# Optimization experiments

Measured on AMD Instinct MI355X. Metric: run time of the kernel, lower is better.

Reference implementation:

```python
import jax, jax.numpy as jnp
import numpy as np

B, T, C = 32, 512, 1024
H, D = 16, 64
BLOCK_SIZE = 512


def setup_inputs() -> dict:
    key = jax.random.key(0)
    ks = jax.random.split(key, 6)
    s_in = 1.0 / np.sqrt(C)
    return {
        "x": jax.random.normal(ks[0], (B, T, C), dtype=jnp.float32),
        "wq": jax.random.normal(ks[1], (H, C, D), dtype=jnp.float32) * s_in,
        "wk": jax.random.normal(ks[2], (H, C, D), dtype=jnp.float32) * s_in,
        "wv": jax.random.normal(ks[3], (H, C, D), dtype=jnp.float32) * s_in,
        "w_proj": jax.random.normal(ks[4], (C, C), dtype=jnp.float32) * s_in,
        "b_proj": jax.random.normal(ks[5], (C,), dtype=jnp.float32) * 0.01,
    }


def reference(x, wq, wk, wv, w_proj, b_proj):
    b, t, c = x.shape
    # per-head projections (bias=False Linears stacked on head axis)
    q = jnp.einsum("btc,hcd->bhtd", x, wq)
    k = jnp.einsum("btc,hcd->bhtd", x, wk)
    v = jnp.einsum("btc,hcd->bhtd", x, wv)
    # NOTE: original scales by 1/sqrt(C) with C = n_embd, not head_size
    scale = 1.0 / (c ** 0.5)
    scores = jnp.einsum("bhtd,bhsd->bhts", q, k) * scale  # [B,H,T,T]
    causal = jnp.tril(jnp.ones((t, t), dtype=bool))
    scores = jnp.where(causal, scores, jnp.finfo(scores.dtype).min)
    attn = jax.nn.softmax(scores, axis=-1)
    out = jnp.einsum("bhts,bhsd->bhtd", attn, v)
    # concat heads in order -> [B,T,H*D]
    out = out.transpose(0, 2, 1, 3).reshape(b, t, -1)
    # output projection (dropout = identity in eval mode)
    return out @ w_proj + b_proj
```

## Files before the change

kernel.cpp:

```cpp
#include <hip/hip_runtime.h>

typedef unsigned int u32;
typedef unsigned short u16;
typedef __bf16 bf16x8 __attribute__((ext_vector_type(8)));
typedef float f32x4 __attribute__((ext_vector_type(4)));
typedef u16 u16x8 __attribute__((ext_vector_type(8)));
typedef u16 u16x4 __attribute__((ext_vector_type(4)));

#define DEVI static __device__ __forceinline__

DEVI u16 f2bf(float f) {
  union { float f; u32 u; } v; v.f = f;
  return (u16)((v.u + 0x7fffu + ((v.u >> 16) & 1u)) >> 16);
}

DEVI u32 cvtpk(float a, float b) {
  u32 r;
  asm("v_cvt_pk_bf16_f32 %0, %1, %2" : "=v"(r) : "v"(a), "v"(b));
  return r;
}

constexpr long QS_ = 16777216;
constexpr long XB_O    = 0;
constexpr long WQKV_O  = 16777216;
constexpr long Q_O     = 19922944;
constexpr long CTX_O   = 70254592;
constexpr long WPROJ_O = 87031808;

__global__ __launch_bounds__(256) void k_cast_x(const float* __restrict__ x, u16* __restrict__ xb) {
  long i = (long)blockIdx.x * 256 + threadIdx.x;
  const float4* p = (const float4*)(x + i * 8);
  float4 a = p[0], b = p[1];
  u16x8 r;
  r[0]=f2bf(a.x); r[1]=f2bf(a.y); r[2]=f2bf(a.z); r[3]=f2bf(a.w);
  r[4]=f2bf(b.x); r[5]=f2bf(b.y); r[6]=f2bf(b.z); r[7]=f2bf(b.w);
  *(u16x8*)(xb + i * 8) = r;
}

__global__ __launch_bounds__(256) void k_prep_wqkv(const float* __restrict__ wq, const float* __restrict__ wk,
                                                   const float* __restrict__ wv, u16* __restrict__ wt) {
  long o = (long)blockIdx.x * 256 + threadIdx.x;
  int n = (int)(o >> 10), kk = (int)(o & 1023);
  int sel = n >> 10, h = (n >> 6) & 15, d = n & 63;
  const float* W = (sel == 0) ? wq : ((sel == 1) ? wk : wv);
  wt[o] = f2bf(W[((long)h * 1024 + kk) * 64 + d]);
}

__global__ __launch_bounds__(256) void k_prep_wproj(const float* __restrict__ wp, u16* __restrict__ wt) {
  long o = (long)blockIdx.x * 256 + threadIdx.x;
  int n = (int)(o >> 10), kk = (int)(o & 1023);
  wt[o] = f2bf(wp[(long)kk * 1024 + n]);
}

DEVI void gload16(const u16* g, u16* l) {
  __builtin_amdgcn_global_load_lds((const __attribute__((address_space(1))) u32*)g,
                                   (__attribute__((address_space(3))) u32*)l, 16, 0, 0);
}

template <int NN, int EPI>
__global__ __launch_bounds__(512, 2)
void k_gemm(const u16* __restrict__ A, const u16* __restrict__ Bt,
            u16* __restrict__ oq, float* __restrict__ of, const float* __restrict__ bias) {
  __shared__ u16 lds[2][4][8192];

  const int tid = threadIdx.x;
  const int lane = tid & 63;
  const int w = tid >> 6;
  const int wm = w >> 2, wn = w & 3;
  const int lg = lane >> 4, lr = lane & 15;
  const int bht = 2 + (wn >> 1);
  const int bn0 = (wn & 1) * 4;

  constexpr int NBN = NN / 256;
  const int nwg = gridDim.x;
  const int swz = ((int)blockIdx.x & 7) * (nwg >> 3) + ((int)blockIdx.x >> 3);
  const long m0 = (long)(swz / NBN) * 256, n0 = (long)(swz % NBN) * 256;

  int srcoff[2];
  #pragma unroll
  for (int r2 = 0; r2 < 2; ++r2) {
    int s = r2 * 8 + w;
    int mi = s >> 1, ks = s & 1;
    int rowl = mi * 16 + (lane >> 2);
    int colu = ks * 32 + (((lane & 3) * 8) ^ (((lane >> 5) & 1) * 16));
    srcoff[r2] = rowl * 1024 + colu;
  }
  const int fo = lr * 32 + ((lg * 8) ^ (((lr >> 3) & 1) * 16));

  const u16* At  = A  + m0 * 1024;
  const u16* Bt2 = Bt + n0 * 1024;

  f32x4 acc[8][4] = {};
  bf16x8 aq[2][2][2];
  bf16x8 bfr[4][2];

#define STAGE(buf_, ht_, gbase_)                                               \
  { _Pragma("unroll") for (int r_ = 0; r_ < 2; ++r_)                           \
      gload16((gbase_) + srcoff[r_], &lds[buf_][ht_][r_ * 4096 + w * 512]); }

#define LDS_AQ(set_, buf_, q_)                                                 \
  { _Pragma("unroll") for (int i_ = 0; i_ < 2; ++i_)                           \
    _Pragma("unroll") for (int ks_ = 0; ks_ < 2; ++ks_)                        \
      aq[set_][i_][ks_] = *(const bf16x8*)&lds[buf_][wm][(((q_)*2 + i_) * 2 + ks_) * 512 + fo]; }

#define LDS_BF(buf_, lo_)                                                      \
  { _Pragma("unroll") for (int j_ = 0; j_ < 2; ++j_)                           \
    _Pragma("unroll") for (int ks_ = 0; ks_ < 2; ++ks_)                        \
      bfr[(lo_) + j_][ks_] = *(const bf16x8*)&lds[buf_][bht][((bn0 + (lo_) + j_) * 2 + ks_) * 512 + fo]; }

#define QUAD8(set_, q_, lo_)                                                   \
  { __builtin_amdgcn_s_setprio(1);                                             \
    _Pragma("unroll") for (int ks_ = 0; ks_ < 2; ++ks_)                        \
    _Pragma("unroll") for (int i_ = 0; i_ < 2; ++i_)                           \
    _Pragma("unroll") for (int j_ = 0; j_ < 2; ++j_)                           \
      acc[(q_)*2 + i_][(lo_) + j_] = __builtin_amdgcn_mfma_f32_16x16x32_bf16(  \
          aq[set_][i_][ks_], bfr[(lo_) + j_][ks_], acc[(q_)*2 + i_][(lo_) + j_], 0, 0, 0); \
    __builtin_amdgcn_s_setprio(0); }

#define BARF() { asm volatile("s_barrier" ::: "memory"); }

  STAGE(0, 0, At);
  STAGE(0, 1, At + 131072);
  STAGE(0, 2, Bt2);
  STAGE(0, 3, Bt2 + 131072);
  STAGE(1, 0, At + 64);
  STAGE(1, 1, At + 131072 + 64);
  STAGE(1, 2, Bt2 + 64);
  STAGE(1, 3, Bt2 + 131072 + 64);
  asm volatile("s_waitcnt vmcnt(8)" ::: "memory");
  BARF();
  LDS_AQ(0, 0, 0);
  LDS_BF(0, 0);

  #pragma unroll 1
  for (int t = 0; t < 16; ++t) {
    const int buf = t & 1;
    LDS_BF(buf, 2);
    LDS_AQ(1, buf, 1);
    QUAD8(0, 0, 0);
    BARF();
    QUAD8(0, 0, 2);
    BARF();
    LDS_AQ(0, buf, 2);
    if (t + 2 < 16) { STAGE(buf, 2, Bt2 + (t + 2) * 64); STAGE(buf, 3, Bt2 + 131072 + (t + 2) * 64); }
    QUAD8(1, 1, 0);
    BARF();
    QUAD8(1, 1, 2);
    BARF();
    LDS_AQ(1, buf, 3);
    QUAD8(0, 2, 0);
    BARF();
    QUAD8(0, 2, 2);
    asm volatile("s_waitcnt lgkmcnt(0)" ::: "memory");
    __builtin_amdgcn_sched_barrier(0);
    BARF();
    if (t + 2 < 16) { STAGE(buf, 0, At + (t + 2) * 64); STAGE(buf, 1, At + 131072 + (t + 2) * 64); }
    QUAD8(1, 3, 0);
    BARF();
    if (t < 14)       { asm volatile("s_waitcnt vmcnt(8)" ::: "memory"); }
    else if (t == 14) { asm volatile("s_waitcnt vmcnt(0)" ::: "memory"); }
    BARF();
    if (t + 1 < 16) {
      LDS_AQ(0, buf ^ 1, 0);
      LDS_BF(buf ^ 1, 0);
    }
    QUAD8(1, 3, 2);
    BARF();
  }

  if constexpr (EPI == 0) {
    #pragma unroll
    for (int mi = 0; mi < 8; ++mi) {
      int grow = (int)m0 + wm * 128 + mi * 16 + lg * 4;
      int b = grow >> 9, t0 = grow & 511;
      #pragma unroll
      for (int ni = 0; ni < 4; ++ni) {
        int gcol = (int)n0 + wn * 64 + ni * 16 + lr;
        int sel = gcol >> 10, h = (gcol >> 6) & 15, d = gcol & 63;
        u16* dst = oq + (long)sel * QS_ + (((long)(b * 16 + h) * 512 + t0) * 64 + d);
        #pragma unroll
        for (int r = 0; r < 4; ++r) dst[r * 64] = f2bf(acc[mi][ni][r]);
      }
    }
  } else {
    float bv[4];
    #pragma unroll
    for (int ni = 0; ni < 4; ++ni) bv[ni] = bias[(int)n0 + wn * 64 + ni * 16 + lr];
    #pragma unroll
    for (int mi = 0; mi < 8; ++mi) {
      int grow = (int)m0 + wm * 128 + mi * 16 + lg * 4;
      #pragma unroll
      for (int ni = 0; ni < 4; ++ni) {
        int gcol = (int)n0 + wn * 64 + ni * 16 + lr;
        #pragma unroll
        for (int r = 0; r < 4; ++r)
          of[(long)(grow + r) * NN + gcol] = acc[mi][ni][r] + bv[ni];
      }
    }
  }
#undef STAGE
#undef LDS_AQ
#undef LDS_BF
#undef QUAD8
#undef BARF
}

__global__ __launch_bounds__(256, 3)
void k_attn(const u16* __restrict__ Qp, const u16* __restrict__ Kp,
            const u16* __restrict__ Vp, u16* __restrict__ ctx) {
  __shared__ u16 k_lds[2][64 * 72];
  __shared__ u16 vt_lds[2][64 * 72];

  const int bid = blockIdx.x;
  const int qi = 3 - (bid >> 9);
  const int bh = bid & 511;
  const int tid = threadIdx.x, lane = tid & 63, w = tid >> 6;
  const int lg = lane >> 4, lr = lane & 15;
  const long base = (long)bh * (512 * 64);

  const int q0 = qi * 128 + w * 32;

  bf16x8 qf[2][2];
  #pragma unroll
  for (int mt = 0; mt < 2; ++mt)
    #pragma unroll
    for (int k2 = 0; k2 < 2; ++k2)
      qf[mt][k2] = *(const bf16x8*)(Qp + base + (long)(q0 + mt * 16 + lr) * 64 + k2 * 32 + lg * 8);

  f32x4 o[2][4] = {};
  float ms[2] = {-1e30f, -1e30f};
  float ls[2] = {0.f, 0.f};

  const int nch = (qi + 1) * 2;
  int srow[2], scol[2], cslot[2];
  #pragma unroll
  for (int i = 0; i < 2; ++i) {
    int s = i * 256 + tid;
    srow[i] = s >> 3; scol[i] = s & 7;
    int sr = srow[i];
    cslot[i] = ((sr >> 5) << 5) + (((sr >> 2) & 3) << 3) + (((sr >> 4) & 1) << 2) + (sr & 3);
  }

  uint4 kreg[2], vreg[2];
  auto loadch = [&](int c) {
    #pragma unroll
    for (int i = 0; i < 2; ++i) {
      long go = base + (long)(c * 64 + srow[i]) * 64 + scol[i] * 8;
      kreg[i] = *(const uint4*)(Kp + go);
      vreg[i] = *(const uint4*)(Vp + go);
    }
  };
  auto writech = [&](int bsel) {
    #pragma unroll
    for (int i = 0; i < 2; ++i) {
      *(uint4*)&k_lds[bsel][srow[i] * 72 + scol[i] * 8] = kreg[i];
      union { uint4 v; u16 s[8]; } t; t.v = vreg[i];
      #pragma unroll
      for (int j = 0; j < 8; ++j)
        vt_lds[bsel][(scol[i] * 8 + j) * 72 + cslot[i]] = t.s[j];
    }
  };

  loadch(0);
  writech(0);
  loadch(1);
  __syncthreads();

  const float sc = 0.045084220027780106f;

  #pragma unroll 1
  for (int c = 0; c < nch; ++c) {
    const int bsel = c & 1;
    if (c + 1 < nch) writech(bsel ^ 1);
    if (c + 2 < nch) loadch(c + 2);

    if (c * 64 <= q0 + 31) {
      const bool full = (c * 64 + 63 <= q0);
      f32x4 st[2][4] = {};
      bf16x8 kf2[4][2];
      #pragma unroll
      for (int nt = 0; nt < 4; ++nt)
        #pragma unroll
        for (int k2 = 0; k2 < 2; ++k2)
          kf2[nt][k2] = *(const bf16x8*)&k_lds[bsel][(nt * 16 + lr) * 72 + k2 * 32 + lg * 8];
      __builtin_amdgcn_s_setprio(1);
      #pragma unroll
      for (int k2 = 0; k2 < 2; ++k2)
        #pragma unroll
        for (int mt = 0; mt < 2; ++mt)
          #pragma unroll
          for (int nt = 0; nt < 4; ++nt)
            st[mt][nt] = __builtin_amdgcn_mfma_f32_16x16x32_bf16(kf2[nt][k2], qf[mt][k2], st[mt][nt], 0, 0, 0);
      __builtin_amdgcn_s_setprio(0);

      u32 pkw[2][4][2];
      #pragma unroll
      for (int mt = 0; mt < 2; ++mt) {
        const int q = q0 + mt * 16 + lr;
        if (!full) {
          #pragma unroll
          for (int nt = 0; nt < 4; ++nt)
            #pragma unroll
            for (int r = 0; r < 4; ++r) {
              int s_ = c * 64 + nt * 16 + lg * 4 + r;
              st[mt][nt][r] = (s_ <= q) ? st[mt][nt][r] : -1e30f;
            }
        }
        float mx = st[mt][0][0];
        #pragma unroll
        for (int nt = 0; nt < 4; ++nt)
          #pragma unroll
          for (int r = 0; r < 4; ++r) mx = fmaxf(mx, st[mt][nt][r]);
        mx = fmaxf(mx, __shfl_xor(mx, 16));
        mx = fmaxf(mx, __shfl_xor(mx, 32));
        const float mnew = fmaxf(ms[mt], mx);
        const float alpha = exp2f((ms[mt] - mnew) * sc);
        ms[mt] = mnew;
        const float msc = mnew * sc;
        float ps = 0.f;
        float p[4][4];
        #pragma unroll
        for (int nt = 0; nt < 4; ++nt)
          #pragma unroll
          for (int r = 0; r < 4; ++r) {
            float pv = exp2f(fmaf(st[mt][nt][r], sc, -msc));
            p[nt][r] = pv;
            ps += pv;
          }
        ps += __shfl_xor(ps, 16);
        ps += __shfl_xor(ps, 32);
        ls[mt] = ls[mt] * alpha + ps;
        #pragma unroll
        for (int nt = 0; nt < 4; ++nt) {
          pkw[mt][nt][0] = cvtpk(p[nt][0], p[nt][1]);
          pkw[mt][nt][1] = cvtpk(p[nt][2], p[nt][3]);
        }
        #pragma unroll
        for (int dt = 0; dt < 4; ++dt) o[mt][dt] *= alpha;
      }

      bf16x8 vf2[4][2];
      #pragma unroll
      for (int dt = 0; dt < 4; ++dt)
        #pragma unroll
        for (int k2 = 0; k2 < 2; ++k2)
          vf2[dt][k2] = *(const bf16x8*)&vt_lds[bsel][(dt * 16 + lr) * 72 + k2 * 32 + lg * 8];
      __builtin_amdgcn_s_setprio(1);
      #pragma unroll
      for (int k2 = 0; k2 < 2; ++k2)
        #pragma unroll
        for (int mt = 0; mt < 2; ++mt) {
          union { u32 w4[4]; bf16x8 v; } pb;
          pb.w4[0] = pkw[mt][2 * k2][0];
          pb.w4[1] = pkw[mt][2 * k2][1];
          pb.w4[2] = pkw[mt][2 * k2 + 1][0];
          pb.w4[3] = pkw[mt][2 * k2 + 1][1];
          #pragma unroll
          for (int dt = 0; dt < 4; ++dt)
            o[mt][dt] = __builtin_amdgcn_mfma_f32_16x16x32_bf16(vf2[dt][k2], pb.v, o[mt][dt], 0, 0, 0);
        }
      __builtin_amdgcn_s_setprio(0);
    }
    __syncthreads();
  }

  const int b = bh >> 4, h = bh & 15;
  #pragma unroll
  for (int mt = 0; mt < 2; ++mt) {
    const int t = q0 + mt * 16 + lr;
    const float inv = 1.0f / ls[mt];
    #pragma unroll
    for (int dt = 0; dt < 4; ++dt) {
      u16x4 pk4;
      #pragma unroll
      for (int r = 0; r < 4; ++r) pk4[r] = f2bf(o[mt][dt][r] * inv);
      *(u16x4*)(ctx + ((long)(b * 512 + t)) * 1024 + h * 64 + dt * 16 + lg * 4) = pk4;
    }
  }
}

extern "C" void kernel_launch(void* const* d_in, const int* in_sizes, int n_in,
                              void* d_out, int out_size, void* d_ws, size_t ws_size,
                              hipStream_t stream) {
  const float* x  = (const float*)d_in[0];
  const float* wq = (const float*)d_in[1];
  const float* wk = (const float*)d_in[2];
  const float* wv = (const float*)d_in[3];
  const float* wp = (const float*)d_in[4];
  const float* bp = (const float*)d_in[5];
  float* out = (float*)d_out;
  u16* ws = (u16*)d_ws;

  u16* XB    = ws + XB_O;
  u16* WQKV  = ws + WQKV_O;
  u16* Qb    = ws + Q_O;
  u16* CTX   = ws + CTX_O;
  u16* WPROJ = ws + WPROJ_O;

  k_cast_x<<<8192, 256, 0, stream>>>(x, XB);
  k_prep_wqkv<<<12288, 256, 0, stream>>>(wq, wk, wv, WQKV);
  k_prep_wproj<<<4096, 256, 0, stream>>>(wp, WPROJ);
  k_gemm<3072, 0><<<(16384 / 256) * (3072 / 256), 512, 0, stream>>>(XB, WQKV, Qb, nullptr, nullptr);
  k_attn<<<2048, 256, 0, stream>>>(Qb, Qb + QS_, Qb + 2 * QS_, CTX);
  k_gemm<1024, 1><<<(16384 / 256) * (1024 / 256), 512, 0, stream>>>(CTX, WPROJ, nullptr, out, bp);
}
```

Baseline: 250.7 us.

## Software-pipeline attention PV step, defer softmax rescale, fuse prep kernels

The three cast/transpose prep kernels are merged into one launch, which removes two kernel launches. In the attention kernel, the P·V MFMA for chunk c-1 now runs after the QK MFMA of chunk c, so matrix work overlaps the softmax math. The max/alpha rescale of the output accumulator is skipped when the new max rises by at most a threshold, in the style of FA4 lazy rescaling. The K/V LDS write now sits between two barriers, which adds a sync per chunk, and the lazy rescale risks exp overflow only within that bounded threshold.

```diff
diff --git a/kernel.cpp b/kernel.cpp
--- a/kernel.cpp
+++ b/kernel.cpp
@@ -27,29 +27,31 @@
 constexpr long CTX_O   = 70254592;
 constexpr long WPROJ_O = 87031808;
 
-__global__ __launch_bounds__(256) void k_cast_x(const float* __restrict__ x, u16* __restrict__ xb) {
-  long i = (long)blockIdx.x * 256 + threadIdx.x;
-  const float4* p = (const float4*)(x + i * 8);
-  float4 a = p[0], b = p[1];
-  u16x8 r;
-  r[0]=f2bf(a.x); r[1]=f2bf(a.y); r[2]=f2bf(a.z); r[3]=f2bf(a.w);
-  r[4]=f2bf(b.x); r[5]=f2bf(b.y); r[6]=f2bf(b.z); r[7]=f2bf(b.w);
-  *(u16x8*)(xb + i * 8) = r;
-}
-
-__global__ __launch_bounds__(256) void k_prep_wqkv(const float* __restrict__ wq, const float* __restrict__ wk,
-                                                   const float* __restrict__ wv, u16* __restrict__ wt) {
-  long o = (long)blockIdx.x * 256 + threadIdx.x;
-  int n = (int)(o >> 10), kk = (int)(o & 1023);
-  int sel = n >> 10, h = (n >> 6) & 15, d = n & 63;
-  const float* W = (sel == 0) ? wq : ((sel == 1) ? wk : wv);
-  wt[o] = f2bf(W[((long)h * 1024 + kk) * 64 + d]);
-}
-
-__global__ __launch_bounds__(256) void k_prep_wproj(const float* __restrict__ wp, u16* __restrict__ wt) {
-  long o = (long)blockIdx.x * 256 + threadIdx.x;
-  int n = (int)(o >> 10), kk = (int)(o & 1023);
-  wt[o] = f2bf(wp[(long)kk * 1024 + n]);
+__global__ __launch_bounds__(256) void k_prep_all(const float* __restrict__ x,
+                                                  const float* __restrict__ wq,
+                                                  const float* __restrict__ wk,
+                                                  const float* __restrict__ wv,
+                                                  const float* __restrict__ wp,
+                                                  u16* __restrict__ ws) {
+  long id = (long)blockIdx.x * 256 + threadIdx.x;
+  if (id < 2097152) {
+    const float4* p = (const float4*)(x + id * 8);
+    float4 a = p[0], b = p[1];
+    u16x8 r;
+    r[0]=f2bf(a.x); r[1]=f2bf(a.y); r[2]=f2bf(a.z); r[3]=f2bf(a.w);
+    r[4]=f2bf(b.x); r[5]=f2bf(b.y); r[6]=f2bf(b.z); r[7]=f2bf(b.w);
+    *(u16x8*)(ws + XB_O + id * 8) = r;
+  } else if (id < 2097152 + 3145728) {
+    long o = id - 2097152;
+    int n = (int)(o >> 10), kk = (int)(o & 1023);
+    int sel = n >> 10, h = (n >> 6) & 15, d = n & 63;
+    const float* W = (sel == 0) ? wq : ((sel == 1) ? wk : wv);
+    ws[WQKV_O + o] = f2bf(W[((long)h * 1024 + kk) * 64 + d]);
+  } else {
+    long o = id - 2097152 - 3145728;
+    int n = (int)(o >> 10), kk = (int)(o & 1023);
+    ws[WPROJ_O + o] = f2bf(wp[(long)kk * 1024 + n]);
+  }
 }
 
 DEVI void gload16(const u16* g, u16* l) {
@@ -230,6 +232,7 @@
   f32x4 o[2][4] = {};
   float ms[2] = {-1e30f, -1e30f};
   float ls[2] = {0.f, 0.f};
+  u32 pkw[2][4][2];
 
   const int nch = (qi + 1) * 2;
   int srow[2], scol[2], cslot[2];
@@ -260,6 +263,29 @@
         vt_lds[bsel][(scol[i] * 8 + j) * 72 + cslot[i]] = t.s[j];
     }
   };
+  auto pv_step = [&](int vsel) {
+    bf16x8 vf2[4][2];
+    #pragma unroll
+    for (int dt = 0; dt < 4; ++dt)
+      #pragma unroll
+      for (int k2 = 0; k2 < 2; ++k2)
+        vf2[dt][k2] = *(const bf16x8*)&vt_lds[vsel][(dt * 16 + lr) * 72 + k2 * 32 + lg * 8];
+    __builtin_amdgcn_s_setprio(1);
+    #pragma unroll
+    for (int k2 = 0; k2 < 2; ++k2)
+      #pragma unroll
+      for (int mt = 0; mt < 2; ++mt) {
+        union { u32 w4[4]; bf16x8 v; } pb;
+        pb.w4[0] = pkw[mt][2 * k2][0];
+        pb.w4[1] = pkw[mt][2 * k2][1];
+        pb.w4[2] = pkw[mt][2 * k2 + 1][0];
+        pb.w4[3] = pkw[mt][2 * k2 + 1][1];
+        #pragma unroll
+        for (int dt = 0; dt < 4; ++dt)
+          o[mt][dt] = __builtin_amdgcn_mfma_f32_16x16x32_bf16(vf2[dt][k2], pb.v, o[mt][dt], 0, 0, 0);
+      }
+    __builtin_amdgcn_s_setprio(0);
+  };
 
   loadch(0);
   writech(0);
@@ -271,12 +297,11 @@
   #pragma unroll 1
   for (int c = 0; c < nch; ++c) {
     const int bsel = c & 1;
-    if (c + 1 < nch) writech(bsel ^ 1);
-    if (c + 2 < nch) loadch(c + 2);
-
-    if (c * 64 <= q0 + 31) {
-      const bool full = (c * 64 + 63 <= q0);
-      f32x4 st[2][4] = {};
+    const bool doQK = (c * 64 <= q0 + 31);
+    const bool doPV = (c >= 1) && ((c - 1) * 64 <= q0 + 31);
+
+    f32x4 st[2][4] = {};
+    if (doQK) {
       bf16x8 kf2[4][2];
       #pragma unroll
       for (int nt = 0; nt < 4; ++nt)
@@ -292,8 +317,12 @@
           for (int nt = 0; nt < 4; ++nt)
             st[mt][nt] = __builtin_amdgcn_mfma_f32_16x16x32_bf16(kf2[nt][k2], qf[mt][k2], st[mt][nt], 0, 0, 0);
       __builtin_amdgcn_s_setprio(0);
-
-      u32 pkw[2][4][2];
+    }
+
+    if (doPV) pv_step(bsel ^ 1);
+
+    if (doQK) {
+      const bool full = (c * 64 + 63 <= q0);
       #pragma unroll
       for (int mt = 0; mt < 2; ++mt) {
         const int q = q0 + mt * 16 + lr;
@@ -313,10 +342,16 @@
           for (int r = 0; r < 4; ++r) mx = fmaxf(mx, st[mt][nt][r]);
         mx = fmaxf(mx, __shfl_xor(mx, 16));
         mx = fmaxf(mx, __shfl_xor(mx, 32));
-        const float mnew = fmaxf(ms[mt], mx);
-        const float alpha = exp2f((ms[mt] - mnew) * sc);
-        ms[mt] = mnew;
-        const float msc = mnew * sc;
+        bool defer = (mx - ms[mt]) * sc <= 8.0f;
+        if (!__all(defer)) {
+          const float mnew = fmaxf(ms[mt], mx);
+          const float alpha = exp2f((ms[mt] - mnew) * sc);
+          ms[mt] = mnew;
+          ls[mt] *= alpha;
+          #pragma unroll
+          for (int dt = 0; dt < 4; ++dt) o[mt][dt] *= alpha;
+        }
+        const float msc = ms[mt] * sc;
         float ps = 0.f;
         float p[4][4];
         #pragma unroll
@@ -329,40 +364,22 @@
           }
         ps += __shfl_xor(ps, 16);
         ps += __shfl_xor(ps, 32);
-        ls[mt] = ls[mt] * alpha + ps;
+        ls[mt] += ps;
         #pragma unroll
         for (int nt = 0; nt < 4; ++nt) {
           pkw[mt][nt][0] = cvtpk(p[nt][0], p[nt][1]);
           pkw[mt][nt][1] = cvtpk(p[nt][2], p[nt][3]);
         }
-        #pragma unroll
-        for (int dt = 0; dt < 4; ++dt) o[mt][dt] *= alpha;
       }
-
-      bf16x8 vf2[4][2];
-      #pragma unroll
-      for (int dt = 0; dt < 4; ++dt)
-        #pragma unroll
-        for (int k2 = 0; k2 < 2; ++k2)
-          vf2[dt][k2] = *(const bf16x8*)&vt_lds[bsel][(dt * 16 + lr) * 72 + k2 * 32 + lg * 8];
-      __builtin_amdgcn_s_setprio(1);
-      #pragma unroll
-      for (int k2 = 0; k2 < 2; ++k2)
-        #pragma unroll
-        for (int mt = 0; mt < 2; ++mt) {
-          union { u32 w4[4]; bf16x8 v; } pb;
-          pb.w4[0] = pkw[mt][2 * k2][0];
-          pb.w4[1] = pkw[mt][2 * k2][1];
-          pb.w4[2] = pkw[mt][2 * k2 + 1][0];
-          pb.w4[3] = pkw[mt][2 * k2 + 1][1];
-          #pragma unroll
-          for (int dt = 0; dt < 4; ++dt)
-            o[mt][dt] = __builtin_amdgcn_mfma_f32_16x16x32_bf16(vf2[dt][k2], pb.v, o[mt][dt], 0, 0, 0);
-        }
-      __builtin_amdgcn_s_setprio(0);
-    }
+    }
+
     __syncthreads();
-  }
+    if (c + 1 < nch) writech(bsel ^ 1);
+    if (c + 2 < nch) loadch(c + 2);
+    __syncthreads();
+  }
+
+  if ((nch - 1) * 64 <= q0 + 31) pv_step((nch - 1) & 1);
 
   const int b = bh >> 4, h = bh & 15;
   #pragma unroll
@@ -397,9 +414,7 @@
   u16* CTX   = ws + CTX_O;
   u16* WPROJ = ws + WPROJ_O;
 
-  k_cast_x<<<8192, 256, 0, stream>>>(x, XB);
-  k_prep_wqkv<<<12288, 256, 0, stream>>>(wq, wk, wv, WQKV);
-  k_prep_wproj<<<4096, 256, 0, stream>>>(wp, WPROJ);
+  k_prep_all<<<24576, 256, 0, stream>>>(x, wq, wk, wv, wp, ws);
   k_gemm<3072, 0><<<(16384 / 256) * (3072 / 256), 512, 0, stream>>>(XB, WQKV, Qb, nullptr, nullptr);
   k_attn<<<2048, 256, 0, stream>>>(Qb, Qb + QS_, Qb + 2 * QS_, CTX);
   k_gemm<1024, 1><<<(16384 / 256) * (1024 / 256), 512, 0, stream>>>(CTX, WPROJ, nullptr, out, bp);
```

New measurement: 248.9 us. No clear change (-0.7%).
